# Kernel optimization log

Hardware: AMD Instinct MI355X
Metric: run time of the kernel (lower is better)

Reference implementation:

```python
import jax, jax.numpy as jnp
import numpy as np

DIM = 128
EXPAND = 2
INTERNAL = DIM * EXPAND  # 256
MAX_SEQ = 2048
BATCH = 32
GATE_DECAY = 3.0


def _gated_cell(x, Wa, ba, Wi, bi, g):
    # x: [B,S,D]; Wa,Wi: [E,D]; ba,bi,g: [E]
    pa = jnp.einsum('bsd,ed->bse', x, Wa) + ba          # projected activation
    pi = jnp.einsum('bsd,ed->bse', x, Wi) + bi          # projected input
    reset_gate = jax.nn.sigmoid(pa)
    input_gate = jax.nn.sigmoid(pi)
    alpha = jax.nn.sigmoid(g)                           # [E]
    a = alpha / jnp.power(GATE_DECAY, reset_gate)       # adaptive alpha [B,S,E]
    u = jnp.sqrt(1.0 - a * a) * (input_gate * pi)       # per-step input [B,S,E]

    def step(h, au):
        a_t, u_t = au
        h = a_t * h + u_t
        return h, h

    h0 = jnp.zeros((x.shape[0], Wa.shape[0]), x.dtype)
    _, ys = jax.lax.scan(step, h0, (a.transpose(1, 0, 2), u.transpose(1, 0, 2)))
    return ys.transpose(1, 0, 2)                        # [B,S,E]


def _recency_weights(seq_len, dtype):
    w = jnp.exp(jnp.linspace(0.0, 3.0, MAX_SEQ))[:seq_len]
    return w.astype(dtype).reshape(1, -1, 1)


def setup_inputs() -> dict:
    key = jax.random.key(0)
    ks = jax.random.split(key, 12)
    std = 1.0 / np.sqrt(DIM)  # kaiming fan_in linear
    lo = float(np.log(0.9 / 0.1))
    hi = float(np.log(0.999 / 0.001))
    d = {
        'x': jax.random.normal(ks[0], (BATCH, MAX_SEQ, DIM), jnp.float32),
        'Wa_u': jax.random.normal(ks[1], (INTERNAL, DIM), jnp.float32) * std,
        'ba_u': jnp.zeros((INTERNAL,), jnp.float32),
        'Wi_u': jax.random.normal(ks[2], (INTERNAL, DIM), jnp.float32) * std,
        'bi_u': jnp.zeros((INTERNAL,), jnp.float32),
        'g_u': jax.random.uniform(ks[3], (INTERNAL,), jnp.float32, lo, hi),
        'Wa_w': jax.random.normal(ks[4], (INTERNAL, DIM), jnp.float32) * std,
        'ba_w': jnp.zeros((INTERNAL,), jnp.float32),
        'Wi_w': jax.random.normal(ks[5], (INTERNAL, DIM), jnp.float32) * std,
        'bi_w': jnp.zeros((INTERNAL,), jnp.float32),
        'g_w': jax.random.uniform(ks[6], (INTERNAL,), jnp.float32, lo, hi),
        'Wf': jax.random.normal(ks[7], (DIM, 4 * DIM), jnp.float32) * (1.0 / np.sqrt(4 * DIM)),
        'bf': jnp.zeros((DIM,), jnp.float32),
    }
    return d


def reference(x, Wa_u, ba_u, Wi_u, bi_u, g_u, Wa_w, ba_w, Wi_w, bi_w, g_w, Wf, bf):
    unweighted = _gated_cell(x, Wa_u, ba_u, Wi_u, bi_u, g_u)          # [B,S,2D]
    xw = x * _recency_weights(x.shape[1], x.dtype)
    weighted = _gated_cell(xw, Wa_w, ba_w, Wi_w, bi_w, g_w)           # [B,S,2D]
    combined = jnp.concatenate([unweighted, weighted], axis=-1)       # [B,S,4D]
    return jnp.einsum('bsf,df->bsd', combined, Wf) + bf               # [B,S,D]
```

## Files before the change

### kernel.cpp

```cpp
#include <hip/hip_runtime.h>
#include <hip/hip_fp16.h>
#include <cstddef>
#include <cstdint>

#define DIM 128
#define SEQ 2048
#define NB 32
#define NCH 512
#define NROWS (NB * SEQ)

typedef _Float16 half8 __attribute__((ext_vector_type(8)));
typedef float    f32x4 __attribute__((ext_vector_type(4)));

#define CMB_BYTES ((size_t)NROWS * NCH * 2)
#define WFG_OFF   CMB_BYTES
#define WFG_BYTES ((size_t)NCH * DIM * 2)
#define WS_NEEDED (WFG_OFF + WFG_BYTES)

__device__ __forceinline__ float sigf(float v) {
    return 1.0f / (1.0f + __expf(-v));
}

__global__ void k0_wfg(const float* __restrict__ Wf, _Float16* __restrict__ Wfg) {
    int o = blockIdx.x * 256 + threadIdx.x;
    int j    = o & 7;
    int lane = (o >> 3) & 63;
    int q    = lane >> 4, n16 = lane & 15;
    int ct   = (o >> 9) & 7;
    int ks   = (o >> 12) & 1;
    int kb   = o >> 13;
    int k = kb * 64 + ks * 32 + q * 8 + j;
    int n = ct * 16 + n16;
    Wfg[o] = (_Float16)Wf[n * NCH + k];
}

__global__ __launch_bounds__(256, 2) void kfused(
        const float* __restrict__ x,
        const float* __restrict__ Wa_u, const float* __restrict__ ba_u,
        const float* __restrict__ Wi_u, const float* __restrict__ bi_u,
        const float* __restrict__ g_u,
        const float* __restrict__ Wa_w, const float* __restrict__ ba_w,
        const float* __restrict__ Wi_w, const float* __restrict__ bi_w,
        const float* __restrict__ g_w,
        _Float16* __restrict__ cmb) {
    __shared__ _Float16 xs[64][136];
    __shared__ float2   seg[16][33];
    __shared__ float    pref[16][33];
    __shared__ float    carry[32];
    __shared__ _Float16 hbuf[64][40];

    const int tid  = threadIdx.x;
    const int lane = tid & 63;
    const int w    = tid >> 6;
    const int quad = lane >> 4;
    const int n16  = lane & 15;

    const int b  = blockIdx.x;
    const int cg = blockIdx.y;
    const int p  = cg >> 3;
    const int ebase = (cg & 7) * 32;

    const float* Wa  = p ? Wa_w : Wa_u;
    const float* Wi  = p ? Wi_w : Wi_u;
    const float* bap = p ? ba_w : ba_u;
    const float* bip = p ? bi_w : bi_u;
    const float* gp  = p ? g_w  : g_u;

    half8 bf[4][4];
#pragma unroll
    for (int ks = 0; ks < 4; ++ks)
#pragma unroll
        for (int nt = 0; nt < 4; ++nt) {
            int e = ebase + (nt & 1) * 16 + n16;
            const float* Wp = (nt >> 1) ? Wi : Wa;
            const float* src = Wp + (size_t)e * DIM + ks * 32 + quad * 8;
            float4 v0 = *(const float4*)src;
            float4 v1 = *(const float4*)(src + 4);
            half8 hv;
            hv[0] = (_Float16)v0.x; hv[1] = (_Float16)v0.y;
            hv[2] = (_Float16)v0.z; hv[3] = (_Float16)v0.w;
            hv[4] = (_Float16)v1.x; hv[5] = (_Float16)v1.y;
            hv[6] = (_Float16)v1.z; hv[7] = (_Float16)v1.w;
            bf[ks][nt] = hv;
        }

    float rba[2], rbi[2], ral[2];
#pragma unroll
    for (int hh = 0; hh < 2; ++hh) {
        int e = ebase + hh * 16 + n16;
        rba[hh] = bap[e];
        rbi[hh] = bip[e];
        ral[hh] = sigf(gp[e]);
    }

    if (tid < 32) carry[tid] = 0.0f;

    const float* xrow = x + (size_t)b * SEQ * DIM;
    _Float16* cmbb = cmb + (size_t)b * SEQ * NCH + cg * 32;

    __syncthreads();

    for (int t = 0; t < 32; ++t) {
        const int s0 = t * 64;

#pragma unroll
        for (int i = 0; i < 4; ++i) {
            int g = tid + i * 256;
            int r = g >> 4, d8 = g & 15;
            const float* srcx = xrow + (size_t)(s0 + r) * DIM + d8 * 8;
            float4 v0 = *(const float4*)srcx;
            float4 v1 = *(const float4*)(srcx + 4);
            half8 hv;
            hv[0] = (_Float16)v0.x; hv[1] = (_Float16)v0.y;
            hv[2] = (_Float16)v0.z; hv[3] = (_Float16)v0.w;
            hv[4] = (_Float16)v1.x; hv[5] = (_Float16)v1.y;
            hv[6] = (_Float16)v1.z; hv[7] = (_Float16)v1.w;
            *(half8*)&xs[r][d8 * 8] = hv;
        }
        __syncthreads();

        f32x4 acc[4];
#pragma unroll
        for (int nt = 0; nt < 4; ++nt) acc[nt] = (f32x4){0.f, 0.f, 0.f, 0.f};
#pragma unroll
        for (int ks = 0; ks < 4; ++ks) {
            half8 af = *(const half8*)&xs[w * 16 + n16][ks * 32 + quad * 8];
#pragma unroll
            for (int nt = 0; nt < 4; ++nt)
                acc[nt] = __builtin_amdgcn_mfma_f32_16x16x32_f16(af, bf[ks][nt], acc[nt], 0, 0, 0);
        }

        const int sbase = s0 + w * 16 + quad * 4;
        float a_s[2][4], u_s[2][4];
#pragma unroll
        for (int hh = 0; hh < 2; ++hh) {
            float A4 = 1.0f, U4 = 0.0f;
#pragma unroll
            for (int reg = 0; reg < 4; ++reg) {
                float sc = p ? __expf((float)(sbase + reg) * (3.0f / 2047.0f)) : 1.0f;
                float pa = fmaf(acc[hh][reg],     sc, rba[hh]);
                float pi = fmaf(acc[2 + hh][reg], sc, rbi[hh]);
                float rst = sigf(pa);
                float ig  = sigf(pi);
                float a   = ral[hh] * exp2f(-rst * 1.5849625007211562f);
                float u   = sqrtf(fmaxf(1.0f - a * a, 0.0f)) * ig * pi;
                a_s[hh][reg] = a; u_s[hh][reg] = u;
                A4 *= a;
                U4 = fmaf(a, U4, u);
            }
            seg[w * 4 + quad][hh * 16 + n16] = make_float2(A4, U4);
        }
        __syncthreads();

        if (tid < 32) {
            float H = carry[tid];
#pragma unroll
            for (int ts = 0; ts < 16; ++ts) {
                float2 AU = seg[ts][tid];
                pref[ts][tid] = H;
                H = fmaf(AU.x, H, AU.y);
            }
            carry[tid] = H;
        }
        __syncthreads();

#pragma unroll
        for (int hh = 0; hh < 2; ++hh) {
            float h = pref[w * 4 + quad][hh * 16 + n16];
#pragma unroll
            for (int reg = 0; reg < 4; ++reg) {
                h = fmaf(a_s[hh][reg], h, u_s[hh][reg]);
                hbuf[w * 16 + quad * 4 + reg][hh * 16 + n16] = (_Float16)h;
            }
        }
        __syncthreads();

        {
            int row = tid >> 2, part = tid & 3;
            half8 hv = *(const half8*)&hbuf[row][part * 8];
            *(half8*)(cmbb + (size_t)(s0 + row) * NCH + part * 8) = hv;
        }
    }
}

__global__ __launch_bounds__(256, 2) void k3_mfma(
        const _Float16* __restrict__ cmb, const _Float16* __restrict__ Wfg,
        const float* __restrict__ bfv, float* __restrict__ out) {
    __shared__ _Float16 As[16 * 512];
    __shared__ _Float16 Bs[16 * 512];

    const int tid  = threadIdx.x;
    const int lane = tid & 63;
    const int w    = tid >> 6;
    const int row0 = blockIdx.x * 128;
    const int q    = lane >> 4;
    const int nn   = lane & 15;

    f32x4 acc[2][8];
#pragma unroll
    for (int rt = 0; rt < 2; ++rt)
#pragma unroll
        for (int ct = 0; ct < 8; ++ct)
            acc[rt][ct] = (f32x4){0.0f, 0.0f, 0.0f, 0.0f};

    for (int kb = 0; kb < 8; ++kb) {
        const int kc = kb * 64;
#pragma unroll
        for (int i = 0; i < 4; ++i) {
            int f = tid + i * 256;
            int r = f >> 3, k8 = f & 7;
            uint4 v = *(const uint4*)(cmb + (size_t)(row0 + r) * NCH + kc + k8 * 8);
            int rt = r >> 4, m = r & 15, ks = k8 >> 2, qq = k8 & 3;
            *(uint4*)&As[(((rt * 2 + ks) * 64) + qq * 16 + m) * 8] = v;
        }
#pragma unroll
        for (int i = 0; i < 4; ++i) {
            int f = tid + i * 256;
            uint4 v = *(const uint4*)(Wfg + (size_t)kb * 8192 + (size_t)f * 8);
            *(uint4*)&Bs[(size_t)f * 8] = v;
        }
        __syncthreads();

#pragma unroll
        for (int ks = 0; ks < 2; ++ks) {
            half8 a0 = *(const half8*)&As[(((w * 2 + 0) * 2 + ks) * 512) + lane * 8];
            half8 a1 = *(const half8*)&As[(((w * 2 + 1) * 2 + ks) * 512) + lane * 8];
#pragma unroll
            for (int ct = 0; ct < 8; ++ct) {
                half8 bb = *(const half8*)&Bs[((ks * 8 + ct) * 512) + lane * 8];
                acc[0][ct] = __builtin_amdgcn_mfma_f32_16x16x32_f16(a0, bb, acc[0][ct], 0, 0, 0);
                acc[1][ct] = __builtin_amdgcn_mfma_f32_16x16x32_f16(a1, bb, acc[1][ct], 0, 0, 0);
            }
        }
        __syncthreads();
    }

#pragma unroll
    for (int rt = 0; rt < 2; ++rt) {
        int rbase = row0 + w * 32 + rt * 16 + q * 4;
#pragma unroll
        for (int ct = 0; ct < 8; ++ct) {
            int col = ct * 16 + nn;
            float bias = bfv[col];
#pragma unroll
            for (int reg = 0; reg < 4; ++reg)
                out[(size_t)(rbase + reg) * DIM + col] = acc[rt][ct][reg] + bias;
        }
    }
}

extern "C" void kernel_launch(void* const* d_in, const int* in_sizes, int n_in,
                              void* d_out, int out_size, void* d_ws, size_t ws_size,
                              hipStream_t stream) {
    if (ws_size < WS_NEEDED) return;

    const float* x    = (const float*)d_in[0];
    const float* Wa_u = (const float*)d_in[1];
    const float* ba_u = (const float*)d_in[2];
    const float* Wi_u = (const float*)d_in[3];
    const float* bi_u = (const float*)d_in[4];
    const float* g_u  = (const float*)d_in[5];
    const float* Wa_w = (const float*)d_in[6];
    const float* ba_w = (const float*)d_in[7];
    const float* Wi_w = (const float*)d_in[8];
    const float* bi_w = (const float*)d_in[9];
    const float* g_w  = (const float*)d_in[10];
    const float* Wf   = (const float*)d_in[11];
    const float* bfv  = (const float*)d_in[12];
    float* out = (float*)d_out;

    char* ws = (char*)d_ws;
    _Float16* cmb = (_Float16*)ws;
    _Float16* Wfg = (_Float16*)(ws + WFG_OFF);

    hipLaunchKernelGGL(k0_wfg, dim3(256), dim3(256), 0, stream, Wf, Wfg);
    hipLaunchKernelGGL(kfused, dim3(32, 16), dim3(256), 0, stream,
                       x, Wa_u, ba_u, Wi_u, bi_u, g_u,
                       Wa_w, ba_w, Wi_w, bi_w, g_w, cmb);
    hipLaunchKernelGGL(k3_mfma, dim3(512), dim3(256), 0, stream,
                       cmb, Wfg, bfv, out);
}
```

Before: 219.2 us.

## Restructure gated-cell kernel: 512 threads, register-prefetched x, weights in LDS

The fused recurrence kernel now runs 512 threads that cover 128 timesteps per iteration. Each thread loads its own x fragment straight into registers and prefetches the next tile during the epilogue, which removes the shared-memory staging of x and one barrier. The projection weights move from registers into LDS to relieve register pressure under the new launch bounds. The recency scale is now a running product instead of a per-element exp, and hidden states are written directly to global memory as scattered 2-byte stores rather than through an LDS transpose. The serial prefix scan over segments doubles in length, and the k0 weight-conversion kernel now does eight elements per thread.

```diff
diff --git a/kernel.cpp b/kernel.cpp
--- a/kernel.cpp
+++ b/kernel.cpp
@@ -22,19 +22,23 @@
 }
 
 __global__ void k0_wfg(const float* __restrict__ Wf, _Float16* __restrict__ Wfg) {
-    int o = blockIdx.x * 256 + threadIdx.x;
-    int j    = o & 7;
-    int lane = (o >> 3) & 63;
-    int q    = lane >> 4, n16 = lane & 15;
-    int ct   = (o >> 9) & 7;
-    int ks   = (o >> 12) & 1;
-    int kb   = o >> 13;
-    int k = kb * 64 + ks * 32 + q * 8 + j;
-    int n = ct * 16 + n16;
-    Wfg[o] = (_Float16)Wf[n * NCH + k];
-}
-
-__global__ __launch_bounds__(256, 2) void kfused(
+    int t = blockIdx.x * 256 + threadIdx.x;
+#pragma unroll
+    for (int i = 0; i < 8; ++i) {
+        int o = t * 8 + i;
+        int j    = o & 7;
+        int lane = (o >> 3) & 63;
+        int q    = lane >> 4, n16 = lane & 15;
+        int ct   = (o >> 9) & 7;
+        int ks   = (o >> 12) & 1;
+        int kb   = o >> 13;
+        int k = kb * 64 + ks * 32 + q * 8 + j;
+        int n = ct * 16 + n16;
+        Wfg[o] = (_Float16)Wf[n * NCH + k];
+    }
+}
+
+__global__ __launch_bounds__(512, 4) void kfused(
         const float* __restrict__ x,
         const float* __restrict__ Wa_u, const float* __restrict__ ba_u,
         const float* __restrict__ Wi_u, const float* __restrict__ bi_u,
@@ -43,11 +47,10 @@
         const float* __restrict__ Wi_w, const float* __restrict__ bi_w,
         const float* __restrict__ g_w,
         _Float16* __restrict__ cmb) {
-    __shared__ _Float16 xs[64][136];
-    __shared__ float2   seg[16][33];
-    __shared__ float    pref[16][33];
+    __shared__ _Float16 Bs[8192];
+    __shared__ float2   seg[32][33];
+    __shared__ float    pref[32][33];
     __shared__ float    carry[32];
-    __shared__ _Float16 hbuf[64][40];
 
     const int tid  = threadIdx.x;
     const int lane = tid & 63;
@@ -66,80 +69,103 @@
     const float* bip = p ? bi_w : bi_u;
     const float* gp  = p ? g_w  : g_u;
 
-    half8 bf[4][4];
-#pragma unroll
-    for (int ks = 0; ks < 4; ++ks)
-#pragma unroll
-        for (int nt = 0; nt < 4; ++nt) {
-            int e = ebase + (nt & 1) * 16 + n16;
-            const float* Wp = (nt >> 1) ? Wi : Wa;
-            const float* src = Wp + (size_t)e * DIM + ks * 32 + quad * 8;
-            float4 v0 = *(const float4*)src;
-            float4 v1 = *(const float4*)(src + 4);
+    for (int sl = tid; sl < 1024; sl += 512) {
+        int l  = sl & 63;
+        int nt = (sl >> 6) & 3;
+        int ks = sl >> 8;
+        int qq = l >> 4, nn = l & 15;
+        int e = ebase + (nt & 1) * 16 + nn;
+        const float* Wp = (nt >> 1) ? Wi : Wa;
+        const float* src = Wp + (size_t)e * DIM + ks * 32 + qq * 8;
+        float4 v0 = *(const float4*)src;
+        float4 v1 = *(const float4*)(src + 4);
+        half8 hv;
+        hv[0] = (_Float16)v0.x; hv[1] = (_Float16)v0.y;
+        hv[2] = (_Float16)v0.z; hv[3] = (_Float16)v0.w;
+        hv[4] = (_Float16)v1.x; hv[5] = (_Float16)v1.y;
+        hv[6] = (_Float16)v1.z; hv[7] = (_Float16)v1.w;
+        *(half8*)&Bs[sl * 8] = hv;
+    }
+
+    float rba[2], rbi[2], ral[2];
+#pragma unroll
+    for (int hh = 0; hh < 2; ++hh) {
+        int e = ebase + hh * 16 + n16;
+        rba[hh] = bap[e];
+        rbi[hh] = bip[e];
+        ral[hh] = sigf(gp[e]);
+    }
+    if (tid < 32) carry[tid] = 0.0f;
+
+    float scb = __expf((float)(w * 16 + quad * 4) * (3.0f / 2047.0f));
+    const float r1    = __expf(3.0f / 2047.0f);
+    const float r2    = r1 * r1;
+    const float r3    = r2 * r1;
+    const float cs128 = __expf(128.0f * 3.0f / 2047.0f);
+
+    const float* xbase = x + ((size_t)b * SEQ + (size_t)(w * 16 + n16)) * DIM + quad * 8;
+    _Float16* cmbb = cmb + (size_t)b * SEQ * NCH + cg * 32 + n16;
+
+    __syncthreads();
+
+    float4 xf[8];
+#pragma unroll
+    for (int ks = 0; ks < 4; ++ks) {
+        xf[2 * ks]     = *(const float4*)(xbase + ks * 32);
+        xf[2 * ks + 1] = *(const float4*)(xbase + ks * 32 + 4);
+    }
+
+    for (int t = 0; t < 16; ++t) {
+        const int s0 = t * 128;
+
+        half8 af[4];
+#pragma unroll
+        for (int ks = 0; ks < 4; ++ks) {
+            float4 v0 = xf[2 * ks], v1 = xf[2 * ks + 1];
             half8 hv;
             hv[0] = (_Float16)v0.x; hv[1] = (_Float16)v0.y;
             hv[2] = (_Float16)v0.z; hv[3] = (_Float16)v0.w;
             hv[4] = (_Float16)v1.x; hv[5] = (_Float16)v1.y;
             hv[6] = (_Float16)v1.z; hv[7] = (_Float16)v1.w;
-            bf[ks][nt] = hv;
-        }
-
-    float rba[2], rbi[2], ral[2];
-#pragma unroll
-    for (int hh = 0; hh < 2; ++hh) {
-        int e = ebase + hh * 16 + n16;
-        rba[hh] = bap[e];
-        rbi[hh] = bip[e];
-        ral[hh] = sigf(gp[e]);
-    }
-
-    if (tid < 32) carry[tid] = 0.0f;
-
-    const float* xrow = x + (size_t)b * SEQ * DIM;
-    _Float16* cmbb = cmb + (size_t)b * SEQ * NCH + cg * 32;
-
-    __syncthreads();
-
-    for (int t = 0; t < 32; ++t) {
-        const int s0 = t * 64;
-
-#pragma unroll
-        for (int i = 0; i < 4; ++i) {
-            int g = tid + i * 256;
-            int r = g >> 4, d8 = g & 15;
-            const float* srcx = xrow + (size_t)(s0 + r) * DIM + d8 * 8;
-            float4 v0 = *(const float4*)srcx;
-            float4 v1 = *(const float4*)(srcx + 4);
-            half8 hv;
-            hv[0] = (_Float16)v0.x; hv[1] = (_Float16)v0.y;
-            hv[2] = (_Float16)v0.z; hv[3] = (_Float16)v0.w;
-            hv[4] = (_Float16)v1.x; hv[5] = (_Float16)v1.y;
-            hv[6] = (_Float16)v1.z; hv[7] = (_Float16)v1.w;
-            *(half8*)&xs[r][d8 * 8] = hv;
-        }
-        __syncthreads();
+            af[ks] = hv;
+        }
 
         f32x4 acc[4];
 #pragma unroll
         for (int nt = 0; nt < 4; ++nt) acc[nt] = (f32x4){0.f, 0.f, 0.f, 0.f};
 #pragma unroll
         for (int ks = 0; ks < 4; ++ks) {
-            half8 af = *(const half8*)&xs[w * 16 + n16][ks * 32 + quad * 8];
-#pragma unroll
-            for (int nt = 0; nt < 4; ++nt)
-                acc[nt] = __builtin_amdgcn_mfma_f32_16x16x32_f16(af, bf[ks][nt], acc[nt], 0, 0, 0);
-        }
-
-        const int sbase = s0 + w * 16 + quad * 4;
+            half8 a = af[ks];
+#pragma unroll
+            for (int nt = 0; nt < 4; ++nt) {
+                half8 bb = *(const half8*)&Bs[(ks * 256 + nt * 64 + lane) * 8];
+                acc[nt] = __builtin_amdgcn_mfma_f32_16x16x32_f16(a, bb, acc[nt], 0, 0, 0);
+            }
+        }
+
+        {
+            int tn = (t + 1) & 15;
+            const float* ab = xbase + (size_t)tn * 128 * DIM;
+#pragma unroll
+            for (int ks = 0; ks < 4; ++ks) {
+                xf[2 * ks]     = *(const float4*)(ab + ks * 32);
+                xf[2 * ks + 1] = *(const float4*)(ab + ks * 32 + 4);
+            }
+        }
+
+        float sc[4];
+        if (p) { sc[0] = scb; sc[1] = scb * r1; sc[2] = scb * r2; sc[3] = scb * r3; }
+        else   { sc[0] = sc[1] = sc[2] = sc[3] = 1.0f; }
+        scb *= cs128;
+
         float a_s[2][4], u_s[2][4];
 #pragma unroll
         for (int hh = 0; hh < 2; ++hh) {
             float A4 = 1.0f, U4 = 0.0f;
 #pragma unroll
             for (int reg = 0; reg < 4; ++reg) {
-                float sc = p ? __expf((float)(sbase + reg) * (3.0f / 2047.0f)) : 1.0f;
-                float pa = fmaf(acc[hh][reg],     sc, rba[hh]);
-                float pi = fmaf(acc[2 + hh][reg], sc, rbi[hh]);
+                float pa = fmaf(acc[hh][reg],     sc[reg], rba[hh]);
+                float pi = fmaf(acc[2 + hh][reg], sc[reg], rbi[hh]);
                 float rst = sigf(pa);
                 float ig  = sigf(pi);
                 float a   = ral[hh] * exp2f(-rst * 1.5849625007211562f);
@@ -155,7 +181,7 @@
         if (tid < 32) {
             float H = carry[tid];
 #pragma unroll
-            for (int ts = 0; ts < 16; ++ts) {
+            for (int ts = 0; ts < 32; ++ts) {
                 float2 AU = seg[ts][tid];
                 pref[ts][tid] = H;
                 H = fmaf(AU.x, H, AU.y);
@@ -167,18 +193,12 @@
 #pragma unroll
         for (int hh = 0; hh < 2; ++hh) {
             float h = pref[w * 4 + quad][hh * 16 + n16];
+            _Float16* dst = cmbb + (size_t)(s0 + w * 16 + quad * 4) * NCH + hh * 16;
 #pragma unroll
             for (int reg = 0; reg < 4; ++reg) {
                 h = fmaf(a_s[hh][reg], h, u_s[hh][reg]);
-                hbuf[w * 16 + quad * 4 + reg][hh * 16 + n16] = (_Float16)h;
-            }
-        }
-        __syncthreads();
-
-        {
-            int row = tid >> 2, part = tid & 3;
-            half8 hv = *(const half8*)&hbuf[row][part * 8];
-            *(half8*)(cmbb + (size_t)(s0 + row) * NCH + part * 8) = hv;
+                dst[(size_t)reg * NCH] = (_Float16)h;
+            }
         }
     }
 }
@@ -273,8 +293,8 @@
     _Float16* cmb = (_Float16*)ws;
     _Float16* Wfg = (_Float16*)(ws + WFG_OFF);
 
-    hipLaunchKernelGGL(k0_wfg, dim3(256), dim3(256), 0, stream, Wf, Wfg);
-    hipLaunchKernelGGL(kfused, dim3(32, 16), dim3(256), 0, stream,
+    hipLaunchKernelGGL(k0_wfg, dim3(32), dim3(256), 0, stream, Wf, Wfg);
+    hipLaunchKernelGGL(kfused, dim3(32, 16), dim3(512), 0, stream,
                        x, Wa_u, ba_u, Wi_u, bi_u, g_u,
                        Wa_w, ba_w, Wi_w, bi_w, g_w, cmb);
     hipLaunchKernelGGL(k3_mfma, dim3(512), dim3(256), 0, stream,
```

Result: faster. 204.9 us (-6.5%).
